# Kernel optimization log

Measured on AMD Instinct MI355X. Metric: run time of the kernel, lower is better.

Reference implementation:

```python
import jax, jax.numpy as jnp
import numpy as np

HIDDEN = 4096
N_HEADS = 32
N_KV_HEADS = 8
HEAD_SIZE = HIDDEN // N_HEADS  # 128
ROPE_THETA = 10000.0
SEQ_LEN = 1024
BATCH = 4


def setup_inputs() -> dict:
    key = jax.random.key(0)
    k1, k2, k3 = jax.random.split(key, 3)
    scale = 1.0 / np.sqrt(HIDDEN)
    hidden_states = jax.random.normal(k1, (BATCH * SEQ_LEN, HIDDEN), dtype=jnp.float32)
    w_qkv = jax.random.normal(k2, ((N_HEADS + 2 * N_KV_HEADS) * HEAD_SIZE, HIDDEN), dtype=jnp.float32) * scale
    w_o = jax.random.normal(k3, (HIDDEN, N_HEADS * HEAD_SIZE), dtype=jnp.float32) * scale
    return {"hidden_states": hidden_states, "w_qkv": w_qkv, "w_o": w_o, "seq_len": SEQ_LEN}


def _rope(x, pos, theta):
    # x: [B, S, H, D]; pos: [S] absolute positions; rotate-half (LLAMA/NeoX) style
    d = x.shape[-1]
    inv_freq = 1.0 / (theta ** (jnp.arange(0, d, 2, dtype=jnp.float32) / d))  # [D/2]
    ang = pos.astype(jnp.float32)[:, None] * inv_freq[None, :]  # [S, D/2]
    cos = jnp.cos(ang)[None, :, None, :]
    sin = jnp.sin(ang)[None, :, None, :]
    x1, x2 = jnp.split(x, 2, axis=-1)
    return jnp.concatenate([x1 * cos - x2 * sin, x2 * cos + x1 * sin], axis=-1)


def reference(hidden_states, w_qkv, w_o, seq_len):
    total, hidden = hidden_states.shape
    B = total // seq_len
    hd = HEAD_SIZE
    # fused QKV projection (bias-free), split like the torch module
    qkv = hidden_states @ w_qkv.T  # [T, (H+2K)*hd]
    q, k, v = jnp.split(qkv, [N_HEADS * hd, (N_HEADS + N_KV_HEADS) * hd], axis=1)
    q = q.reshape(B, seq_len, N_HEADS, hd)
    k = k.reshape(B, seq_len, N_KV_HEADS, hd)
    v = v.reshape(B, seq_len, N_KV_HEADS, hd)
    # inline RoPE (ROPE_LLAMA) on q and k at absolute positions
    pos = jnp.arange(seq_len)
    q = _rope(q, pos, ROPE_THETA)
    k = _rope(k, pos, ROPE_THETA)
    # GQA: map each q head to its kv head (kv_head_mapping = repeat_interleave)
    groups = N_HEADS // N_KV_HEADS
    k = jnp.repeat(k, groups, axis=2)  # [B, S, H, hd]
    v = jnp.repeat(v, groups, axis=2)
    scale = hd ** -0.5
    scores = jnp.einsum('bqhd,bkhd->bhqk', q, k) * scale  # [B, H, S, S]
    causal = jnp.tril(jnp.ones((seq_len, seq_len), dtype=bool))
    scores = jnp.where(causal[None, None], scores, jnp.finfo(scores.dtype).min)
    probs = jax.nn.softmax(scores, axis=-1)
    attn = jnp.einsum('bhqk,bkhd->bqhd', probs, v).reshape(total, N_HEADS * hd)
    return attn @ w_o.T  # [T, hidden]
```

## Files before the change

kernel.cpp:

```cpp
#include <hip/hip_runtime.h>


typedef short bf16x8 __attribute__((ext_vector_type(8)));
typedef short bf16x4 __attribute__((ext_vector_type(4)));
typedef float floatx4 __attribute__((ext_vector_type(4)));
typedef unsigned short u16x4 __attribute__((ext_vector_type(4)));

__device__ __forceinline__ unsigned short f2bf(float f) {
  unsigned u = __float_as_uint(f);
  u += 0x7FFFu + ((u >> 16) & 1u);
  return (unsigned short)(u >> 16);
}
__device__ __forceinline__ float bf2f(unsigned short h) {
  return __uint_as_float(((unsigned)h) << 16);
}

__device__ __forceinline__ void async16(const void* g, void* l) {
  __builtin_amdgcn_global_load_lds(
      (const __attribute__((address_space(1))) unsigned int*)g,
      (__attribute__((address_space(3))) unsigned int*)l, 16, 0, 0);
}

__global__ void cvt_f32_bf16(const float4* __restrict__ in,
                             u16x4* __restrict__ out, int n4) {
  int i = blockIdx.x * 256 + threadIdx.x;
  if (i < n4) {
    float4 v = in[i];
    u16x4 o;
    o.x = f2bf(v.x); o.y = f2bf(v.y); o.z = f2bf(v.z); o.w = f2bf(v.w);
    out[i] = o;
  }
}

template <int OUT_BF16>
__global__ __launch_bounds__(512, 2) void gemm256(
    const unsigned short* __restrict__ A, const unsigned short* __restrict__ B,
    void* __restrict__ Cout, int M, int N, int K) {
  __shared__ __align__(16) unsigned short As[4][8192];
  __shared__ __align__(16) unsigned short Bs[4][8192];
  const int tid = threadIdx.x;
  const int wave = tid >> 6, lane = tid & 63;
  const int wm = wave >> 2, wn = wave & 3;
  const int l16 = lane & 15, c4 = lane >> 4;

  const int nwg = gridDim.x * gridDim.y;
  int bid = blockIdx.y * gridDim.x + blockIdx.x;
  bid = (bid & 7) * (nwg >> 3) + (bid >> 3);
  const int bm = (bid / gridDim.x) << 8, bn = (bid % gridDim.x) << 8;

  int afOff[8], bfOff[4];
#pragma unroll
  for (int mi = 0; mi < 8; ++mi) {
    int r = wm * 128 + mi * 16 + l16;
    int pr = r >> 1, l8 = ((r & 1) << 2) | c4;
    afOff[mi] = pr * 128 + ((l8 ^ (pr & 7)) << 4);
  }
#pragma unroll
  for (int ni = 0; ni < 4; ++ni) {
    int r = wn * 64 + ni * 16 + l16;
    int pr = r >> 1, l8 = ((r & 1) << 2) | c4;
    bfOff[ni] = pr * 128 + ((l8 ^ (pr & 7)) << 4);
  }

  const int sp = lane >> 3;
  const int l8s = (lane & 7) ^ sp;
  const int so = l8s >> 2, sc = (l8s & 3) << 3;
  const unsigned short* aS0 = A + (size_t)(bm + wave * 16 + sp * 2 + so) * K + sc;
  const unsigned short* aS1 = A + (size_t)(bm + (wave + 8) * 16 + sp * 2 + so) * K + sc;
  const unsigned short* bS0 = B + (size_t)(bn + wave * 16 + sp * 2 + so) * K + sc;
  const unsigned short* bS1 = B + (size_t)(bn + (wave + 8) * 16 + sp * 2 + so) * K + sc;
  const int dst0 = wave * 1024, dst1 = (wave + 8) * 1024;

  floatx4 acc[8][4];
#pragma unroll
  for (int mi = 0; mi < 8; ++mi)
#pragma unroll
    for (int ni = 0; ni < 4; ++ni) acc[mi][ni] = (floatx4){0.f, 0.f, 0.f, 0.f};

  const int NT = K >> 5;
  async16(aS0, (char*)As[0] + dst0);
  async16(aS1, (char*)As[0] + dst1);
  async16(bS0, (char*)Bs[0] + dst0);
  async16(bS1, (char*)Bs[0] + dst1);
  async16(aS0 + 32, (char*)As[1] + dst0);
  async16(aS1 + 32, (char*)As[1] + dst1);
  async16(bS0 + 32, (char*)Bs[1] + dst0);
  async16(bS1 + 32, (char*)Bs[1] + dst1);
  asm volatile("s_waitcnt vmcnt(4)" ::: "memory");
  __builtin_amdgcn_s_barrier();

  bf16x8 afq0[4], afq1[4], bfcA[4], bfcB[4];
#pragma unroll
  for (int i = 0; i < 4; ++i)
    afq0[i] = *(const bf16x8*)((const char*)As[0] + afOff[i]);
#pragma unroll
  for (int i = 0; i < 4; ++i)
    bfcA[i] = *(const bf16x8*)((const char*)Bs[0] + bfOff[i]);

  size_t koff = 64;

#define KTILE(T, BC, BN_)                                                     \
  {                                                                           \
    const char* aB = (const char*)As[(T) & 3];                                \
    const char* aN = (const char*)As[((T) + 1) & 3];                          \
    const char* bN = (const char*)Bs[((T) + 1) & 3];                          \
    char* aD = (char*)As[((T) + 2) & 3];                                      \
    char* bD = (char*)Bs[((T) + 2) & 3];                                      \
    _Pragma("unroll") for (int i = 0; i < 4; ++i)                             \
        afq1[i] = *(const bf16x8*)(aB + afOff[4 + i]);                        \
    async16(aS0 + koff, aD + dst0);                                           \
    async16(aS1 + koff, aD + dst1);                                           \
    __builtin_amdgcn_s_barrier();                                             \
    __builtin_amdgcn_s_setprio(1);                                            \
    _Pragma("unroll") for (int mi = 0; mi < 4; ++mi)                          \
        _Pragma("unroll") for (int ni = 0; ni < 4; ++ni)                      \
            acc[mi][ni] = __builtin_amdgcn_mfma_f32_16x16x32_bf16(            \
                afq0[mi], BC[ni], acc[mi][ni], 0, 0, 0);                      \
    __builtin_amdgcn_s_setprio(0);                                            \
    asm volatile("s_waitcnt vmcnt(2)" ::: "memory");   \
    __builtin_amdgcn_s_barrier();                     \
    _Pragma("unroll") for (int i = 0; i < 4; ++i)                             \
        afq0[i] = *(const bf16x8*)(aN + afOff[i]);                            \
    _Pragma("unroll") for (int i = 0; i < 4; ++i)                             \
        BN_[i] = *(const bf16x8*)(bN + bfOff[i]);                             \
    async16(bS0 + koff, bD + dst0);                                           \
    async16(bS1 + koff, bD + dst1);                                           \
    __builtin_amdgcn_s_barrier();                                             \
    __builtin_amdgcn_s_setprio(1);                                            \
    _Pragma("unroll") for (int mi = 0; mi < 4; ++mi)                          \
        _Pragma("unroll") for (int ni = 0; ni < 4; ++ni)                      \
            acc[4 + mi][ni] = __builtin_amdgcn_mfma_f32_16x16x32_bf16(        \
                afq1[mi], BC[ni], acc[4 + mi][ni], 0, 0, 0);                  \
    __builtin_amdgcn_s_setprio(0);                                            \
    __builtin_amdgcn_s_barrier();                                             \
    koff += 32;                                                               \
  }

  for (int t = 0; t < NT; t += 2) {
    KTILE(t, bfcA, bfcB);
    KTILE(t + 1, bfcB, bfcA);
  }
#undef KTILE

  const int col0 = bn + wn * 64 + l16;
#pragma unroll
  for (int mi = 0; mi < 8; ++mi) {
    const int row0 = bm + wm * 128 + mi * 16 + c4 * 4;
#pragma unroll
    for (int ni = 0; ni < 4; ++ni)
#pragma unroll
      for (int r = 0; r < 4; ++r) {
        if (OUT_BF16)
          ((unsigned short*)Cout)[(size_t)(row0 + r) * N + col0 + ni * 16] =
              f2bf(acc[mi][ni][r]);
        else
          ((float*)Cout)[(size_t)(row0 + r) * N + col0 + ni * 16] =
              acc[mi][ni][r];
      }
  }
}

__global__ void rope_k_kernel(unsigned short* __restrict__ qkv) {
  const int t = blockIdx.x;
  const int s = t & 1023;
  const int head = 32 + blockIdx.y * 4 + (threadIdx.x >> 6);
  const int d = threadIdx.x & 63;
  unsigned short* p = qkv + (size_t)t * 6144 + head * 128;
  float x1 = bf2f(p[d]), x2 = bf2f(p[d + 64]);
  float inv_freq = exp2f((float)d * -0.20762050593046015f);
  float ang = (float)s * inv_freq;
  float c, sn;
  __sincosf(ang, &sn, &c);
  p[d] = f2bf(x1 * c - x2 * sn);
  p[d + 64] = f2bf(x2 * c + x1 * sn);
}

__global__ __launch_bounds__(256, 3) void flash_attn(
    const unsigned short* __restrict__ qkv, unsigned short* __restrict__ aout) {
  const int pr = blockIdx.x;
  const int h = blockIdx.y, b = blockIdx.z;
  const int kh = h >> 2;
  const int tid = threadIdx.x;
  const int wave = tid >> 6, lane = tid & 63;
  const int quad = lane >> 4, l16 = lane & 15;

  __shared__ __align__(16) unsigned short Ks[64][136];
  __shared__ __align__(16) unsigned short Vt[128][68];
  __shared__ __align__(16) unsigned short Ps[64][68];

  const int krow = tid >> 4, kcol = (tid & 15) << 3;
  const int vrb = (tid & 15) << 2, vcol = (tid >> 4) << 3;
  const unsigned short* kp = qkv + (size_t)(b << 10) * 6144 + 4096 + kh * 128;
  const unsigned short* vp = qkv + (size_t)(b << 10) * 6144 + 5120 + kh * 128;

  for (int half = 0; half < 2; ++half) {
    const int qt = half ? pr : 15 - pr;
    const int q0 = qt << 6;

    bf16x8 qf[4];
    {
      const int qrow = q0 + wave * 16 + l16;
      const unsigned short* qp =
          qkv + (size_t)((b << 10) + qrow) * 6144 + h * 128 + quad * 8;
#pragma unroll
      for (int ks = 0; ks < 4; ++ks) qf[ks] = *(const bf16x8*)(qp + ks * 32);
      const float pos = (float)qrow;
      const float scale = 0.08838834764831845f;
#pragma unroll
      for (int ks = 0; ks < 2; ++ks)
#pragma unroll
        for (int e = 0; e < 8; ++e) {
          int d = ks * 32 + quad * 8 + e;
          float ang = pos * exp2f((float)d * -0.20762050593046015f);
          float c, sn;
          __sincosf(ang, &sn, &c);
          float x1 = bf2f((unsigned short)qf[ks][e]);
          float x2 = bf2f((unsigned short)qf[ks + 2][e]);
          qf[ks][e] = (short)f2bf((x1 * c - x2 * sn) * scale);
          qf[ks + 2][e] = (short)f2bf((x2 * c + x1 * sn) * scale);
        }
    }

    floatx4 o_acc[8];
#pragma unroll
    for (int i = 0; i < 8; ++i) o_acc[i] = (floatx4){0.f, 0.f, 0.f, 0.f};
    float l_lane[4] = {0.f, 0.f, 0.f, 0.f};

    bf16x8 kreg[4], vreg[4];
#pragma unroll
    for (int j = 0; j < 4; ++j)
      kreg[j] = *(const bf16x8*)(kp + (size_t)(krow + j * 16) * 6144 + kcol);
#pragma unroll
    for (int j = 0; j < 4; ++j)
      vreg[j] = *(const bf16x8*)(vp + (size_t)(vrb + j) * 6144 + vcol);

    for (int t = 0; t <= qt; ++t) {
      __syncthreads();
#pragma unroll
      for (int j = 0; j < 4; ++j)
        *(bf16x8*)&Ks[krow + j * 16][kcol] = kreg[j];
#pragma unroll
      for (int e = 0; e < 8; ++e) {
        bf16x4 w = {vreg[0][e], vreg[1][e], vreg[2][e], vreg[3][e]};
        *(bf16x4*)&Vt[vcol + e][vrb] = w;
      }
      __syncthreads();
      if (t < qt) {
        const size_t nb = (size_t)((t + 1) << 6) * 6144;
#pragma unroll
        for (int j = 0; j < 4; ++j)
          kreg[j] =
              *(const bf16x8*)(kp + nb + (size_t)(krow + j * 16) * 6144 + kcol);
#pragma unroll
        for (int j = 0; j < 4; ++j)
          vreg[j] = *(const bf16x8*)(vp + nb + (size_t)(vrb + j) * 6144 + vcol);
      }

      floatx4 sacc[4];
#pragma unroll
      for (int ni = 0; ni < 4; ++ni) sacc[ni] = (floatx4){0.f, 0.f, 0.f, 0.f};
#pragma unroll
      for (int ks = 0; ks < 4; ++ks)
#pragma unroll
        for (int ni = 0; ni < 4; ++ni) {
          bf16x8 kf = *(const bf16x8*)&Ks[ni * 16 + l16][ks * 32 + quad * 8];
          sacc[ni] = __builtin_amdgcn_mfma_f32_16x16x32_bf16(qf[ks], kf,
                                                             sacc[ni], 0, 0, 0);
        }

      const bool masked = (t == qt);
#pragma unroll
      for (int r = 0; r < 4; ++r) {
        float rs = 0.f;
#pragma unroll
        for (int ni = 0; ni < 4; ++ni) {
          float e = __expf(sacc[ni][r]);
          if (masked && (ni * 16 + l16) > (wave * 16 + quad * 4 + r)) e = 0.f;
          rs += e;
          Ps[wave * 16 + quad * 4 + r][ni * 16 + l16] = f2bf(e);
        }
        l_lane[r] += rs;
      }
      asm volatile("s_waitcnt lgkmcnt(0)" ::: "memory");

#pragma unroll
      for (int ks2 = 0; ks2 < 2; ++ks2) {
        bf16x8 pf = *(const bf16x8*)&Ps[wave * 16 + l16][ks2 * 32 + quad * 8];
#pragma unroll
        for (int n8 = 0; n8 < 8; ++n8) {
          bf16x8 vf = *(const bf16x8*)&Vt[n8 * 16 + l16][ks2 * 32 + quad * 8];
          o_acc[n8] = __builtin_amdgcn_mfma_f32_16x16x32_bf16(pf, vf, o_acc[n8],
                                                              0, 0, 0);
        }
      }
    }

#pragma unroll
    for (int r = 0; r < 4; ++r) {
      float l = l_lane[r];
#pragma unroll
      for (int off = 1; off < 16; off <<= 1) l += __shfl_xor(l, off, 64);
      float inv = 1.0f / l;
      int row = q0 + wave * 16 + quad * 4 + r;
      unsigned short* op = aout + (size_t)((b << 10) + row) * 4096 + h * 128;
#pragma unroll
      for (int n8 = 0; n8 < 8; ++n8)
        op[n8 * 16 + l16] = f2bf(o_acc[n8][r] * inv);
    }
  }
}

extern "C" void kernel_launch(void* const* d_in, const int* in_sizes, int n_in,
                              void* d_out, int out_size, void* d_ws,
                              size_t ws_size, hipStream_t stream) {
  const float* X = (const float*)d_in[0];
  const float* Wqkv = (const float*)d_in[1];
  const float* Wo = (const float*)d_in[2];
  (void)in_sizes; (void)n_in; (void)out_size; (void)ws_size;

  char* ws = (char*)d_ws;
  unsigned short* Wqkvb = (unsigned short*)ws;
  unsigned short* AttnB = (unsigned short*)ws;
  unsigned short* Xb = (unsigned short*)(ws + 50331648);
  unsigned short* Wob = (unsigned short*)(ws + 50331648);
  unsigned short* QKVb = (unsigned short*)(ws + 83886080);

  cvt_f32_bf16<<<16384, 256, 0, stream>>>((const float4*)X, (u16x4*)Xb, 4194304);
  cvt_f32_bf16<<<24576, 256, 0, stream>>>((const float4*)Wqkv, (u16x4*)Wqkvb, 6291456);
  gemm256<1><<<dim3(24, 16), 512, 0, stream>>>(Xb, Wqkvb, QKVb, 4096, 6144, 4096);
  rope_k_kernel<<<dim3(4096, 2), 256, 0, stream>>>(QKVb);
  cvt_f32_bf16<<<16384, 256, 0, stream>>>((const float4*)Wo, (u16x4*)Wob, 4194304);
  flash_attn<<<dim3(8, 32, 4), 256, 0, stream>>>(QKVb, AttnB);
  gemm256<0><<<dim3(16, 16), 512, 0, stream>>>(AttnB, Wob, d_out, 4096, 4096, 4096);
}
```

Before: 655.9 us.

## Split QKV GEMM into two launches, drop tile swizzle, widen bf16 conversion

```diff
diff --git a/kernel.cpp b/kernel.cpp
--- a/kernel.cpp
+++ b/kernel.cpp
@@ -4,7 +4,7 @@
 typedef short bf16x8 __attribute__((ext_vector_type(8)));
 typedef short bf16x4 __attribute__((ext_vector_type(4)));
 typedef float floatx4 __attribute__((ext_vector_type(4)));
-typedef unsigned short u16x4 __attribute__((ext_vector_type(4)));
+typedef unsigned short u16x8 __attribute__((ext_vector_type(8)));
 
 __device__ __forceinline__ unsigned short f2bf(float f) {
   unsigned u = __float_as_uint(f);
@@ -22,12 +22,13 @@
 }
 
 __global__ void cvt_f32_bf16(const float4* __restrict__ in,
-                             u16x4* __restrict__ out, int n4) {
+                             u16x8* __restrict__ out, int n8) {
   int i = blockIdx.x * 256 + threadIdx.x;
-  if (i < n4) {
-    float4 v = in[i];
-    u16x4 o;
-    o.x = f2bf(v.x); o.y = f2bf(v.y); o.z = f2bf(v.z); o.w = f2bf(v.w);
+  if (i < n8) {
+    float4 a = in[2 * i], b = in[2 * i + 1];
+    u16x8 o;
+    o[0] = f2bf(a.x); o[1] = f2bf(a.y); o[2] = f2bf(a.z); o[3] = f2bf(a.w);
+    o[4] = f2bf(b.x); o[5] = f2bf(b.y); o[6] = f2bf(b.z); o[7] = f2bf(b.w);
     out[i] = o;
   }
 }
@@ -35,18 +36,14 @@
 template <int OUT_BF16>
 __global__ __launch_bounds__(512, 2) void gemm256(
     const unsigned short* __restrict__ A, const unsigned short* __restrict__ B,
-    void* __restrict__ Cout, int M, int N, int K) {
+    void* __restrict__ Cout, int M, int N, int K, int n0) {
   __shared__ __align__(16) unsigned short As[4][8192];
   __shared__ __align__(16) unsigned short Bs[4][8192];
   const int tid = threadIdx.x;
   const int wave = tid >> 6, lane = tid & 63;
   const int wm = wave >> 2, wn = wave & 3;
   const int l16 = lane & 15, c4 = lane >> 4;
-
-  const int nwg = gridDim.x * gridDim.y;
-  int bid = blockIdx.y * gridDim.x + blockIdx.x;
-  bid = (bid & 7) * (nwg >> 3) + (bid >> 3);
-  const int bm = (bid / gridDim.x) << 8, bn = (bid % gridDim.x) << 8;
+  const int bm = blockIdx.y << 8, bn = (blockIdx.x << 8) + n0;
 
   int afOff[8], bfOff[4];
 #pragma unroll
@@ -325,11 +322,12 @@
   unsigned short* Wob = (unsigned short*)(ws + 50331648);
   unsigned short* QKVb = (unsigned short*)(ws + 83886080);
 
-  cvt_f32_bf16<<<16384, 256, 0, stream>>>((const float4*)X, (u16x4*)Xb, 4194304);
-  cvt_f32_bf16<<<24576, 256, 0, stream>>>((const float4*)Wqkv, (u16x4*)Wqkvb, 6291456);
-  gemm256<1><<<dim3(24, 16), 512, 0, stream>>>(Xb, Wqkvb, QKVb, 4096, 6144, 4096);
+  cvt_f32_bf16<<<8192, 256, 0, stream>>>((const float4*)X, (u16x8*)Xb, 2097152);
+  cvt_f32_bf16<<<12288, 256, 0, stream>>>((const float4*)Wqkv, (u16x8*)Wqkvb, 3145728);
+  gemm256<1><<<dim3(16, 16), 512, 0, stream>>>(Xb, Wqkvb, QKVb, 4096, 6144, 4096, 0);
+  gemm256<1><<<dim3(8, 16), 512, 0, stream>>>(Xb, Wqkvb, QKVb, 4096, 6144, 4096, 4096);
   rope_k_kernel<<<dim3(4096, 2), 256, 0, stream>>>(QKVb);
-  cvt_f32_bf16<<<16384, 256, 0, stream>>>((const float4*)Wo, (u16x4*)Wob, 4194304);
+  cvt_f32_bf16<<<8192, 256, 0, stream>>>((const float4*)Wo, (u16x8*)Wob, 2097152);
   flash_attn<<<dim3(8, 32, 4), 256, 0, stream>>>(QKVb, AttnB);
-  gemm256<0><<<dim3(16, 16), 512, 0, stream>>>(AttnB, Wob, d_out, 4096, 4096, 4096);
-}
+  gemm256<0><<<dim3(16, 16), 512, 0, stream>>>(AttnB, Wob, d_out, 4096, 4096, 4096, 0);
+}
```

New measurement: 674.7 us. 1.03x slower.
